# Optimization experiments

Hardware: AMD Instinct MI355X
Metric: run time of the kernel (lower is better)

## Reference

```python
import jax, jax.numpy as jnp
import numpy as np

B = 128          # batch
D = 1024         # image_size
K = 100          # timesteps


def setup_inputs() -> dict:
    key = jax.random.key(0)
    kx, kt, ks = jax.random.split(key, 3)
    x = jax.random.normal(kx, (B, D, D), dtype=jnp.float32)
    T = jax.random.normal(kt, (K, D, D), dtype=jnp.float32)
    # timesteps in [1, K], matching torch indexing T[fwd_steps[i] - 1]
    fwd_steps = jax.random.randint(ks, (B,), 1, K + 1, dtype=jnp.int64)
    return {"x": x, "fwd_steps": fwd_steps, "T": T}


def reference(x, fwd_steps, T):
    # Gather the per-sample matrix and do a batched matmul:
    # out[b] = T[fwd_steps[b]-1] @ x[b]
    Tb = T[fwd_steps - 1]                     # [B, D, D]
    return jnp.einsum('bij,bjk->bik', Tb, x)  # [B, D, D]
```

## Files before the change

### kernel.cpp

```cpp
#include <hip/hip_runtime.h>
#include <hip/hip_bf16.h>

#define DDIM 1024
#define BM 128
#define BN 128
#define BK 32
#define LDK 40

typedef __attribute__((ext_vector_type(4))) float floatx4;
typedef __attribute__((ext_vector_type(8))) short shortx8;
typedef __attribute__((ext_vector_type(4))) float floatv4;

static __device__ __forceinline__ short f2bf(float f) {
    union { __bf16 h; short s; } u;
    u.h = (__bf16)f;
    return u.s;
}

__global__ __launch_bounds__(256) void gather_bmm(
    const float* __restrict__ X, const int* __restrict__ steps,
    const float* __restrict__ Tm, float* __restrict__ out)
{
    __shared__ unsigned short As[BM * LDK];
    __shared__ unsigned short Bs[BN * LDK];

    const int tid = threadIdx.x;
    const int bx = blockIdx.x, by = blockIdx.y, b = blockIdx.z;
    const int idx = steps[b] - 1;

    const float* __restrict__ Ta = Tm + (size_t)idx * DDIM * DDIM + (size_t)(by * BM) * DDIM;
    const float* __restrict__ Xb = X + (size_t)b * DDIM * DDIM + bx * BN;
    float* __restrict__ Ob = out + (size_t)b * DDIM * DDIM;

    const int am = tid >> 2;
    const int akq = tid & 3;
    const int nn = tid & 127;
    const int kg = tid >> 7;

    const int wave = tid >> 6, lane = tid & 63;
    const int wm = (wave >> 1) * 64, wn = (wave & 1) * 64;
    const int lrow = lane & 15, quad = lane >> 4;

    floatv4 acc[4][4];
#pragma unroll
    for (int i = 0; i < 4; ++i)
#pragma unroll
        for (int j = 0; j < 4; ++j)
            acc[i][j] = (floatv4){0.f, 0.f, 0.f, 0.f};

    floatx4 aR[2][2];
    float bR[16];

    const float* ap0 = Ta + (size_t)am * DDIM + akq * 8;
    const float* ap1 = ap0 + (size_t)64 * DDIM;
    const float* bp  = Xb + (size_t)(kg * 16) * DDIM + nn;

    aR[0][0] = *(const floatx4*)(ap0);
    aR[0][1] = *(const floatx4*)(ap0 + 4);
    aR[1][0] = *(const floatx4*)(ap1);
    aR[1][1] = *(const floatx4*)(ap1 + 4);
#pragma unroll
    for (int j = 0; j < 16; ++j) bR[j] = bp[(size_t)j * DDIM];

    for (int k0 = 0; k0 < DDIM; k0 += BK) {
        __syncthreads();
#pragma unroll
        for (int i = 0; i < 2; ++i) {
            float t[8];
            *(floatx4*)t = aR[i][0];
            *(floatx4*)(t + 4) = aR[i][1];
            shortx8 v;
#pragma unroll
            for (int e = 0; e < 8; ++e) v[e] = f2bf(t[e]);
            *(shortx8*)&As[(am + i * 64) * LDK + akq * 8] = v;
        }
        {
            shortx8 v0, v1;
#pragma unroll
            for (int e = 0; e < 8; ++e) v0[e] = f2bf(bR[e]);
#pragma unroll
            for (int e = 0; e < 8; ++e) v1[e] = f2bf(bR[e + 8]);
            *(shortx8*)&Bs[nn * LDK + kg * 16] = v0;
            *(shortx8*)&Bs[nn * LDK + kg * 16 + 8] = v1;
        }
        __syncthreads();
        if (k0 + BK < DDIM) {
            const float* a0 = ap0 + k0 + BK;
            const float* a1 = ap1 + k0 + BK;
            aR[0][0] = *(const floatx4*)(a0);
            aR[0][1] = *(const floatx4*)(a0 + 4);
            aR[1][0] = *(const floatx4*)(a1);
            aR[1][1] = *(const floatx4*)(a1 + 4);
            const float* bq = bp + (size_t)(k0 + BK) * DDIM;
#pragma unroll
            for (int j = 0; j < 16; ++j) bR[j] = bq[(size_t)j * DDIM];
        }
        shortx8 af[4], bfrag[4];
#pragma unroll
        for (int i = 0; i < 4; ++i)
            af[i] = *(const shortx8*)&As[(wm + i * 16 + lrow) * LDK + quad * 8];
#pragma unroll
        for (int j = 0; j < 4; ++j)
            bfrag[j] = *(const shortx8*)&Bs[(wn + j * 16 + lrow) * LDK + quad * 8];
#pragma unroll
        for (int i = 0; i < 4; ++i)
#pragma unroll
            for (int j = 0; j < 4; ++j)
                acc[i][j] = __builtin_amdgcn_mfma_f32_16x16x32_bf16(
                    af[i], bfrag[j], acc[i][j], 0, 0, 0);
    }

#pragma unroll
    for (int i = 0; i < 4; ++i) {
        const int row0 = by * BM + wm + i * 16 + quad * 4;
#pragma unroll
        for (int j = 0; j < 4; ++j) {
            const int col = bx * BN + wn + j * 16 + lrow;
#pragma unroll
            for (int r = 0; r < 4; ++r)
                __builtin_nontemporal_store(acc[i][j][r],
                    &Ob[(size_t)(row0 + r) * DDIM + col]);
        }
    }
}

extern "C" void kernel_launch(void* const* d_in, const int* in_sizes, int n_in,
                              void* d_out, int out_size, void* d_ws, size_t ws_size,
                              hipStream_t stream) {
    const float* X     = (const float*)d_in[0];
    const int*   steps = (const int*)d_in[1];
    const float* Tm    = (const float*)d_in[2];
    float* out = (float*)d_out;
    const int nb = in_sizes[1];
    dim3 grid(DDIM / BN, DDIM / BM, nb);
    gather_bmm<<<grid, 256, 0, stream>>>(X, steps, Tm, out);
}
```

Before: 1.506 ms.

## Double-buffer register prefetch two tiles ahead and remap blocks per XCD

Global loads are now prefetched two K-tiles ahead using two alternating register sets, and each load is issued before the second barrier rather than after it, which gives memory latency more time to hide. The grid is flattened to 1D and remapped so that consecutive workgroups of the same batch land on the same XCD, which should improve L2 reuse of the T and X tiles. The extra register set raises VGPR pressure and may lower occupancy.

```diff
diff --git a/kernel.cpp b/kernel.cpp
--- a/kernel.cpp
+++ b/kernel.cpp
@@ -5,6 +5,7 @@
 #define BM 128
 #define BN 128
 #define BK 32
+#define NT (DDIM / BK)
 #define LDK 40
 
 typedef __attribute__((ext_vector_type(4))) float floatx4;
@@ -17,6 +18,52 @@
     return u.s;
 }
 
+#define LOAD_TILE(aR, bR, KT)                                        \
+  { const float* a0_ = ap0 + (KT) * BK;                              \
+    const float* a1_ = ap1 + (KT) * BK;                              \
+    aR[0][0] = *(const floatx4*)(a0_);                               \
+    aR[0][1] = *(const floatx4*)(a0_ + 4);                           \
+    aR[1][0] = *(const floatx4*)(a1_);                               \
+    aR[1][1] = *(const floatx4*)(a1_ + 4);                           \
+    const float* bq_ = bp + (size_t)((KT) * BK) * DDIM;              \
+    _Pragma("unroll")                                                \
+    for (int j = 0; j < 16; ++j) bR[j] = bq_[(size_t)j * DDIM]; }
+
+#define STEP(aR, bR, KN)                                             \
+  { __syncthreads();                                                 \
+    _Pragma("unroll")                                                \
+    for (int i = 0; i < 2; ++i) {                                    \
+      float tt[8];                                                   \
+      *(floatx4*)tt = aR[i][0]; *(floatx4*)(tt + 4) = aR[i][1];      \
+      shortx8 v;                                                     \
+      _Pragma("unroll")                                              \
+      for (int e = 0; e < 8; ++e) v[e] = f2bf(tt[e]);                \
+      *(shortx8*)&As[(am + i * 64) * LDK + akq * 8] = v;             \
+    }                                                                \
+    { shortx8 v0, v1;                                                \
+      _Pragma("unroll")                                              \
+      for (int e = 0; e < 8; ++e) v0[e] = f2bf(bR[e]);               \
+      _Pragma("unroll")                                              \
+      for (int e = 0; e < 8; ++e) v1[e] = f2bf(bR[e + 8]);           \
+      *(shortx8*)&Bs[nn * LDK + kg * 16] = v0;                       \
+      *(shortx8*)&Bs[nn * LDK + kg * 16 + 8] = v1;                   \
+    }                                                                \
+    if ((KN) < NT) LOAD_TILE(aR, bR, KN);                            \
+    __syncthreads();                                                 \
+    shortx8 af_[4], bf_[4];                                          \
+    _Pragma("unroll")                                                \
+    for (int i = 0; i < 4; ++i)                                      \
+      af_[i] = *(const shortx8*)&As[(wm + i * 16 + lrow) * LDK + quad * 8]; \
+    _Pragma("unroll")                                                \
+    for (int j = 0; j < 4; ++j)                                      \
+      bf_[j] = *(const shortx8*)&Bs[(wn + j * 16 + lrow) * LDK + quad * 8]; \
+    _Pragma("unroll")                                                \
+    for (int i = 0; i < 4; ++i)                                      \
+      _Pragma("unroll")                                              \
+      for (int j = 0; j < 4; ++j)                                    \
+        acc[i][j] = __builtin_amdgcn_mfma_f32_16x16x32_bf16(         \
+            af_[i], bf_[j], acc[i][j], 0, 0, 0); }
+
 __global__ __launch_bounds__(256) void gather_bmm(
     const float* __restrict__ X, const int* __restrict__ steps,
     const float* __restrict__ Tm, float* __restrict__ out)
@@ -25,7 +72,16 @@
     __shared__ unsigned short Bs[BN * LDK];
 
     const int tid = threadIdx.x;
-    const int bx = blockIdx.x, by = blockIdx.y, b = blockIdx.z;
+
+    const int nwg = gridDim.x;
+    const int orig = blockIdx.x;
+    const int q = nwg >> 3, r = nwg & 7;
+    const int xcd = orig & 7, pos = orig >> 3;
+    const int wg = (xcd < r ? xcd * (q + 1) : r * (q + 1) + (xcd - r) * q) + pos;
+    const int b  = wg >> 6;
+    const int t6 = wg & 63;
+    const int by = t6 >> 3, bx = t6 & 7;
+
     const int idx = steps[b] - 1;
 
     const float* __restrict__ Ta = Tm + (size_t)idx * DDIM * DDIM + (size_t)(by * BM) * DDIM;
@@ -48,66 +104,19 @@
         for (int j = 0; j < 4; ++j)
             acc[i][j] = (floatv4){0.f, 0.f, 0.f, 0.f};
 
-    floatx4 aR[2][2];
-    float bR[16];
-
     const float* ap0 = Ta + (size_t)am * DDIM + akq * 8;
     const float* ap1 = ap0 + (size_t)64 * DDIM;
     const float* bp  = Xb + (size_t)(kg * 16) * DDIM + nn;
 
-    aR[0][0] = *(const floatx4*)(ap0);
-    aR[0][1] = *(const floatx4*)(ap0 + 4);
-    aR[1][0] = *(const floatx4*)(ap1);
-    aR[1][1] = *(const floatx4*)(ap1 + 4);
-#pragma unroll
-    for (int j = 0; j < 16; ++j) bR[j] = bp[(size_t)j * DDIM];
+    floatx4 aP[2][2], aQ[2][2];
+    float   bP[16],   bQ[16];
 
-    for (int k0 = 0; k0 < DDIM; k0 += BK) {
-        __syncthreads();
-#pragma unroll
-        for (int i = 0; i < 2; ++i) {
-            float t[8];
-            *(floatx4*)t = aR[i][0];
-            *(floatx4*)(t + 4) = aR[i][1];
-            shortx8 v;
-#pragma unroll
-            for (int e = 0; e < 8; ++e) v[e] = f2bf(t[e]);
-            *(shortx8*)&As[(am + i * 64) * LDK + akq * 8] = v;
-        }
-        {
-            shortx8 v0, v1;
-#pragma unroll
-            for (int e = 0; e < 8; ++e) v0[e] = f2bf(bR[e]);
-#pragma unroll
-            for (int e = 0; e < 8; ++e) v1[e] = f2bf(bR[e + 8]);
-            *(shortx8*)&Bs[nn * LDK + kg * 16] = v0;
-            *(shortx8*)&Bs[nn * LDK + kg * 16 + 8] = v1;
-        }
-        __syncthreads();
-        if (k0 + BK < DDIM) {
-            const float* a0 = ap0 + k0 + BK;
-            const float* a1 = ap1 + k0 + BK;
-            aR[0][0] = *(const floatx4*)(a0);
-            aR[0][1] = *(const floatx4*)(a0 + 4);
-            aR[1][0] = *(const floatx4*)(a1);
-            aR[1][1] = *(const floatx4*)(a1 + 4);
-            const float* bq = bp + (size_t)(k0 + BK) * DDIM;
-#pragma unroll
-            for (int j = 0; j < 16; ++j) bR[j] = bq[(size_t)j * DDIM];
-        }
-        shortx8 af[4], bfrag[4];
-#pragma unroll
-        for (int i = 0; i < 4; ++i)
-            af[i] = *(const shortx8*)&As[(wm + i * 16 + lrow) * LDK + quad * 8];
-#pragma unroll
-        for (int j = 0; j < 4; ++j)
-            bfrag[j] = *(const shortx8*)&Bs[(wn + j * 16 + lrow) * LDK + quad * 8];
-#pragma unroll
-        for (int i = 0; i < 4; ++i)
-#pragma unroll
-            for (int j = 0; j < 4; ++j)
-                acc[i][j] = __builtin_amdgcn_mfma_f32_16x16x32_bf16(
-                    af[i], bfrag[j], acc[i][j], 0, 0, 0);
+    LOAD_TILE(aP, bP, 0);
+    LOAD_TILE(aQ, bQ, 1);
+
+    for (int kt = 0; kt < NT; kt += 2) {
+        STEP(aP, bP, kt + 2);
+        STEP(aQ, bQ, kt + 3);
     }
 
 #pragma unroll
@@ -117,9 +126,9 @@
         for (int j = 0; j < 4; ++j) {
             const int col = bx * BN + wn + j * 16 + lrow;
 #pragma unroll
-            for (int r = 0; r < 4; ++r)
-                __builtin_nontemporal_store(acc[i][j][r],
-                    &Ob[(size_t)(row0 + r) * DDIM + col]);
+            for (int rr = 0; rr < 4; ++rr)
+                __builtin_nontemporal_store(acc[i][j][rr],
+                    &Ob[(size_t)(row0 + rr) * DDIM + col]);
         }
     }
 }
@@ -132,6 +141,6 @@
     const float* Tm    = (const float*)d_in[2];
     float* out = (float*)d_out;
     const int nb = in_sizes[1];
-    dim3 grid(DDIM / BN, DDIM / BM, nb);
-    gather_bmm<<<grid, 256, 0, stream>>>(X, steps, Tm, out);
+    const int total = nb * (DDIM / BM) * (DDIM / BN);
+    gather_bmm<<<dim3(total), 256, 0, stream>>>(X, steps, Tm, out);
 }
```

After: 1.436 ms. -4.7%, faster.
